# Performance work log

Measured on AMD Instinct MI355X. Metric: run time of the kernel, lower is better.

The kernel has to match this reference:

```python
import math
import jax, jax.numpy as jnp
import numpy as np

FACTOR = 1  # init factor; top_k = max(1, int(FACTOR * log(L)))


def setup_inputs() -> dict:
    key = jax.random.key(0)
    kq, kk, kv = jax.random.split(key, 3)
    B, L, H, E = 8, 4096, 8, 64
    queries = jax.random.normal(kq, (B, L, H, E), dtype=jnp.float32)
    keys = jax.random.normal(kk, (B, L, H, E), dtype=jnp.float32)
    values = jax.random.normal(kv, (B, L, H, E), dtype=jnp.float32)
    return {"queries": queries, "keys": keys, "values": values}


def reference(queries, keys, values):
    # queries/keys: [B, L, H, E], values: [B, L, H, D] (L == S so no padding branch)
    B, L, H, E = queries.shape
    q = jnp.transpose(queries, (0, 2, 3, 1))  # [B, H, E, L]
    k = jnp.transpose(keys, (0, 2, 3, 1))
    v = jnp.transpose(values, (0, 2, 3, 1))   # [B, H, D, L]

    # FFT-based circular cross-correlation along time axis
    qf = jnp.fft.rfft(q, axis=-1)
    kf = jnp.fft.rfft(k, axis=-1)
    corr = jnp.fft.irfft(qf * jnp.conj(kf), n=L, axis=-1)  # [B, H, E, L]

    # Inference-time delay aggregation (eval path of the module)
    top_k = max(1, int(FACTOR * math.log(L)))
    mean_corr = corr.mean(axis=(1, 2))                      # [B, L]
    w_top, idx_top = jax.lax.top_k(mean_corr, top_k)        # [B, K]
    w = jax.nn.softmax(w_top, axis=-1)                      # [B, K]

    # circular shift: out[..., t] = sum_i w_i * v[..., (t + delay_i) mod L]
    t = jnp.arange(L)
    idx = (t[None, None, :] + idx_top[:, :, None]) % L      # [B, K, L]
    gathered = jnp.take_along_axis(
        v[:, None], idx[:, :, None, None, :], axis=-1
    )                                                       # [B, K, H, D, L]
    agg = jnp.einsum('bkhdl,bk->bhdl', gathered, w)         # [B, H, D, L]
    return jnp.transpose(agg, (0, 3, 1, 2))                 # [B, L, H, D]
```

## Files before the change

kernel.cpp:

```cpp
#include <hip/hip_runtime.h>
#include <math.h>


namespace {
constexpr int LEN  = 4096;
constexpr int HALF = 2048;
constexpr int NCH  = 512;
constexpr int NB   = 8;
constexpr int KTOP = 8;
constexpr int TPB  = 256;
constexpr int CPB  = 8;
constexpr int GPB  = NCH / CPB;
constexpr size_t SF_BYTES = (size_t)NB * LEN * 2 * sizeof(float);
constexpr size_t WI_BYTES = (size_t)NB * KTOP * sizeof(float);
constexpr size_t ZT_OFF   = SF_BYTES + 2 * WI_BYTES;
constexpr size_t ZT_BYTES = (size_t)NB * NCH * LEN * 2 * sizeof(float);
}

__device__ __forceinline__ void fft4096_fwd(float2* __restrict__ bufA,
                                            float2* __restrict__ bufB,
                                            const float2* __restrict__ tw,
                                            int tid)
{
  float2* src = bufA;
  float2* dst = bufB;
  #pragma unroll
  for (int st = 0; st < 12; ++st) {
    const int s = 1 << st;
    #pragma unroll
    for (int r = 0; r < HALF / TPB; ++r) {
      const int j = tid + r * TPB;
      const int q = j & (s - 1);
      const int p = j >> st;
      const float2 a = src[j];
      const float2 b = src[j + HALF];
      const float2 w = tw[j - q];
      const float dx = a.x - b.x, dy = a.y - b.y;
      const int o0 = j + s * p;
      dst[o0]     = make_float2(a.x + b.x, a.y + b.y);
      dst[o0 + s] = make_float2(dx * w.x - dy * w.y, dx * w.y + dy * w.x);
    }
    __syncthreads();
    float2* t_ = src; src = dst; dst = t_;
  }
}

__global__ __launch_bounds__(TPB) void k_transpose(
    const float* __restrict__ qg, const float* __restrict__ kg,
    float2* __restrict__ zt)
{
  __shared__ float2 tile[64 * 65];
  const int bt  = blockIdx.x;
  const int b   = bt >> 9;
  const int t0  = ((bt >> 3) & 63) * 64;
  const int c0  = (bt & 7) * 64;
  const int tid = threadIdx.x;
  const size_t base = (size_t)b * LEN * NCH;

  #pragma unroll
  for (int r = 0; r < 16; ++r) {
    const int idx  = r * TPB + tid;
    const int ch_l = idx & 63;
    const int t_l  = idx >> 6;
    const size_t g = base + (size_t)(t0 + t_l) * NCH + (c0 + ch_l);
    tile[t_l * 65 + ch_l] = make_float2(qg[g], kg[g]);
  }
  __syncthreads();
  #pragma unroll
  for (int r = 0; r < 16; ++r) {
    const int idx  = r * TPB + tid;
    const int t_l  = idx & 63;
    const int ch_l = idx >> 6;
    zt[((size_t)b * NCH + (c0 + ch_l)) * LEN + (t0 + t_l)] =
        tile[t_l * 65 + ch_l];
  }
}

__global__ __launch_bounds__(TPB) void k_fft_corr(
    const float2* __restrict__ zt,
    float* __restrict__ Sf)
{
  __shared__ float2 bufA[LEN];
  __shared__ float2 bufB[LEN];
  __shared__ float2 tw[HALF];
  const int tid = threadIdx.x;
  const int b   = blockIdx.x / GPB;
  const int g   = blockIdx.x % GPB;
  const int ch0 = g * CPB;

  for (int t = tid; t < HALF; t += TPB) {
    float s, c;
    __sincosf((float)t * (float)(-2.0 * M_PI / 4096.0), &s, &c);
    tw[t] = make_float2(c, s);
  }

  float2 acc[LEN / TPB];
  #pragma unroll
  for (int r = 0; r < LEN / TPB; ++r) acc[r] = make_float2(0.f, 0.f);

  for (int cc = 0; cc < CPB; ++cc) {
    const float2* src = zt + ((size_t)b * NCH + (ch0 + cc)) * LEN;
    __syncthreads();
    #pragma unroll
    for (int r = 0; r < LEN / TPB; ++r) {
      const int t = tid + r * TPB;
      bufA[t] = src[t];
    }
    __syncthreads();
    fft4096_fwd(bufA, bufB, tw, tid);
    #pragma unroll
    for (int r = 0; r < LEN / TPB; ++r) {
      const int f = tid + r * TPB;
      const float2 A  = bufA[f];
      float2 Bv = bufA[(LEN - f) & (LEN - 1)];
      Bv.y = -Bv.y;
      const float Sx = A.x + Bv.x, Sy = A.y + Bv.y;
      const float Dx = A.x - Bv.x, Dy = -(A.y - Bv.y);
      const float Mx = Sx * Dx - Sy * Dy;
      const float My = Sx * Dy + Sy * Dx;
      acc[r].x += -0.25f * My;
      acc[r].y +=  0.25f * Mx;
    }
  }
  float* dstp = Sf + (size_t)b * LEN * 2;
  #pragma unroll
  for (int r = 0; r < LEN / TPB; ++r) {
    const int f = tid + r * TPB;
    atomicAdd(&dstp[2 * f],     acc[r].x);
    atomicAdd(&dstp[2 * f + 1], acc[r].y);
  }
}

__global__ __launch_bounds__(TPB) void k_fft_corr_strided(
    const float* __restrict__ qg, const float* __restrict__ kg,
    float* __restrict__ Sf)
{
  __shared__ float2 bufA[LEN];
  __shared__ float2 bufB[LEN];
  __shared__ float2 tw[HALF];
  const int tid = threadIdx.x;
  const int b   = blockIdx.x / GPB;
  const int g   = blockIdx.x % GPB;
  const int ch0 = g * CPB;

  for (int t = tid; t < HALF; t += TPB) {
    float s, c;
    __sincosf((float)t * (float)(-2.0 * M_PI / 4096.0), &s, &c);
    tw[t] = make_float2(c, s);
  }
  float2 acc[LEN / TPB];
  #pragma unroll
  for (int r = 0; r < LEN / TPB; ++r) acc[r] = make_float2(0.f, 0.f);

  const size_t base = (size_t)b * LEN * NCH;
  for (int cc = 0; cc < CPB; ++cc) {
    const int ch = ch0 + cc;
    __syncthreads();
    #pragma unroll
    for (int r = 0; r < LEN / TPB; ++r) {
      const int t = tid + r * TPB;
      const size_t idx = base + (size_t)t * NCH + ch;
      bufA[t] = make_float2(qg[idx], kg[idx]);
    }
    __syncthreads();
    fft4096_fwd(bufA, bufB, tw, tid);
    #pragma unroll
    for (int r = 0; r < LEN / TPB; ++r) {
      const int f = tid + r * TPB;
      const float2 A  = bufA[f];
      float2 Bv = bufA[(LEN - f) & (LEN - 1)];
      Bv.y = -Bv.y;
      const float Sx = A.x + Bv.x, Sy = A.y + Bv.y;
      const float Dx = A.x - Bv.x, Dy = -(A.y - Bv.y);
      const float Mx = Sx * Dx - Sy * Dy;
      const float My = Sx * Dy + Sy * Dx;
      acc[r].x += -0.25f * My;
      acc[r].y +=  0.25f * Mx;
    }
  }
  float* dstp = Sf + (size_t)b * LEN * 2;
  #pragma unroll
  for (int r = 0; r < LEN / TPB; ++r) {
    const int f = tid + r * TPB;
    atomicAdd(&dstp[2 * f],     acc[r].x);
    atomicAdd(&dstp[2 * f + 1], acc[r].y);
  }
}

__global__ __launch_bounds__(TPB) void k_ifft_topk(
    const float* __restrict__ Sf,
    float* __restrict__ wout, int* __restrict__ iout)
{
  __shared__ float2 bufA[LEN];
  __shared__ float2 bufB[LEN];
  __shared__ float2 tw[HALF];
  __shared__ float  R[LEN];
  __shared__ float  rv[TPB];
  __shared__ int    ri[TPB];
  __shared__ float  topv[KTOP];
  __shared__ int    topi[KTOP];
  const int tid = threadIdx.x;
  const int b   = blockIdx.x;

  for (int t = tid; t < HALF; t += TPB) {
    float s, c;
    __sincosf((float)t * (float)(-2.0 * M_PI / 4096.0), &s, &c);
    tw[t] = make_float2(c, s);
  }
  const float* srcp = Sf + (size_t)b * LEN * 2;
  for (int r = 0; r < LEN / TPB; ++r) {
    const int f = tid + r * TPB;
    bufA[f] = make_float2(srcp[2 * f], -srcp[2 * f + 1]);
  }
  __syncthreads();
  fft4096_fwd(bufA, bufB, tw, tid);
  const float scale = 1.0f / (4096.0f * 512.0f);
  for (int r = 0; r < LEN / TPB; ++r) {
    const int f = tid + r * TPB;
    R[f] = bufA[f].x * scale;
  }
  __syncthreads();

  for (int it = 0; it < KTOP; ++it) {
    float best = -INFINITY; int bi = 0;
    for (int r = 0; r < LEN / TPB; ++r) {
      const int f = tid + r * TPB;
      const float v = R[f];
      if (v > best) { best = v; bi = f; }
    }
    rv[tid] = best; ri[tid] = bi;
    __syncthreads();
    for (int off = TPB / 2; off > 0; off >>= 1) {
      if (tid < off && rv[tid + off] > rv[tid]) {
        rv[tid] = rv[tid + off]; ri[tid] = ri[tid + off];
      }
      __syncthreads();
    }
    if (tid == 0) {
      topv[it] = rv[0]; topi[it] = ri[0];
      R[ri[0]] = -INFINITY;
    }
    __syncthreads();
  }
  if (tid == 0) {
    const float m = topv[0];
    float e[KTOP], den = 0.f;
    for (int i = 0; i < KTOP; ++i) { e[i] = expf(topv[i] - m); den += e[i]; }
    for (int i = 0; i < KTOP; ++i) {
      wout[b * KTOP + i] = e[i] / den;
      iout[b * KTOP + i] = topi[i];
    }
  }
}

__global__ __launch_bounds__(256) void k_gather(
    const float4* __restrict__ v, const float* __restrict__ wk,
    const int* __restrict__ ik, float4* __restrict__ out)
{
  __shared__ float sw[KTOP];
  __shared__ int   sidx[KTOP];
  const int b  = blockIdx.x >> 11;
  const int tp = blockIdx.x & 2047;
  if (threadIdx.x < KTOP) {
    sw[threadIdx.x]   = wk[b * KTOP + threadIdx.x];
    sidx[threadIdx.x] = ik[b * KTOP + threadIdx.x];
  }
  __syncthreads();
  const int t = tp * 2 + (threadIdx.x >> 7);
  const int c = threadIdx.x & 127;
  const size_t vbase = (size_t)b * LEN * 128;
  float4 acc = make_float4(0.f, 0.f, 0.f, 0.f);
  #pragma unroll
  for (int i = 0; i < KTOP; ++i) {
    const int st = (t + sidx[i]) & (LEN - 1);
    const float4 x = v[vbase + (size_t)st * 128 + c];
    acc.x += sw[i] * x.x; acc.y += sw[i] * x.y;
    acc.z += sw[i] * x.z; acc.w += sw[i] * x.w;
  }
  out[vbase + (size_t)t * 128 + c] = acc;
}

extern "C" void kernel_launch(void* const* d_in, const int* in_sizes, int n_in,
                              void* d_out, int out_size, void* d_ws, size_t ws_size,
                              hipStream_t stream) {
  const float* q = (const float*)d_in[0];
  const float* k = (const float*)d_in[1];
  const float* v = (const float*)d_in[2];
  float* out = (float*)d_out;

  float*  Sf = (float*)d_ws;
  float*  wk = (float*)((char*)d_ws + SF_BYTES);
  int*    ik = (int*)((char*)d_ws + SF_BYTES + WI_BYTES);
  float2* zt = (float2*)((char*)d_ws + ZT_OFF);

  hipMemsetAsync(d_ws, 0, SF_BYTES, stream);
  if (ws_size >= ZT_OFF + ZT_BYTES) {
    k_transpose<<<NB * 64 * 8, TPB, 0, stream>>>(q, k, zt);
    k_fft_corr<<<NB * GPB, TPB, 0, stream>>>(zt, Sf);
  } else {
    k_fft_corr_strided<<<NB * GPB, TPB, 0, stream>>>(q, k, Sf);
  }
  k_ifft_topk<<<NB, TPB, 0, stream>>>(Sf, wk, ik);
  k_gather<<<NB * 2048, 256, 0, stream>>>((const float4*)v, wk, ik,
                                          (float4*)out);
}
```

Measured before the change: 413.2 us.

## Replace radix-2 Stockham FFT with in-place radix-16 three-pass FFT

```diff
diff --git a/kernel.cpp b/kernel.cpp
--- a/kernel.cpp
+++ b/kernel.cpp
@@ -4,45 +4,117 @@
 
 namespace {
 constexpr int LEN  = 4096;
-constexpr int HALF = 2048;
 constexpr int NCH  = 512;
 constexpr int NB   = 8;
 constexpr int KTOP = 8;
 constexpr int TPB  = 256;
-constexpr int CPB  = 8;
+constexpr int CPB  = 4;
 constexpr int GPB  = NCH / CPB;
 constexpr size_t SF_BYTES = (size_t)NB * LEN * 2 * sizeof(float);
 constexpr size_t WI_BYTES = (size_t)NB * KTOP * sizeof(float);
 constexpr size_t ZT_OFF   = SF_BYTES + 2 * WI_BYTES;
 constexpr size_t ZT_BYTES = (size_t)NB * NCH * LEN * 2 * sizeof(float);
-}
-
-__device__ __forceinline__ void fft4096_fwd(float2* __restrict__ bufA,
-                                            float2* __restrict__ bufB,
-                                            const float2* __restrict__ tw,
-                                            int tid)
-{
-  float2* src = bufA;
-  float2* dst = bufB;
-  #pragma unroll
-  for (int st = 0; st < 12; ++st) {
-    const int s = 1 << st;
-    #pragma unroll
-    for (int r = 0; r < HALF / TPB; ++r) {
-      const int j = tid + r * TPB;
-      const int q = j & (s - 1);
-      const int p = j >> st;
-      const float2 a = src[j];
-      const float2 b = src[j + HALF];
-      const float2 w = tw[j - q];
-      const float dx = a.x - b.x, dy = a.y - b.y;
-      const int o0 = j + s * p;
-      dst[o0]     = make_float2(a.x + b.x, a.y + b.y);
-      dst[o0 + s] = make_float2(dx * w.x - dy * w.y, dx * w.y + dy * w.x);
-    }
-    __syncthreads();
-    float2* t_ = src; src = dst; dst = t_;
-  }
+constexpr int PADN = LEN + (LEN >> 4);
+}
+
+#define PD(i) ((i) + ((i) >> 4))
+
+__device__ __forceinline__ float2 cmul(float2 a, float2 b) {
+  return make_float2(a.x * b.x - a.y * b.y, a.x * b.y + a.y * b.x);
+}
+
+__device__ __forceinline__ void dft16(const float2* __restrict__ a,
+                                      float2* __restrict__ b) {
+  const float C1 = 0.92387953251128674f;
+  const float S1 = 0.38268343236508978f;
+  const float R2 = 0.70710678118654752f;
+  float2 c[4][4];
+  #pragma unroll
+  for (int r0 = 0; r0 < 4; ++r0) {
+    const float2 x0 = a[r0], x1 = a[4 + r0], x2 = a[8 + r0], x3 = a[12 + r0];
+    const float2 s02 = make_float2(x0.x + x2.x, x0.y + x2.y);
+    const float2 d02 = make_float2(x0.x - x2.x, x0.y - x2.y);
+    const float2 s13 = make_float2(x1.x + x3.x, x1.y + x3.y);
+    const float2 d13 = make_float2(x1.x - x3.x, x1.y - x3.y);
+    c[r0][0] = make_float2(s02.x + s13.x, s02.y + s13.y);
+    c[r0][2] = make_float2(s02.x - s13.x, s02.y - s13.y);
+    c[r0][1] = make_float2(d02.x + d13.y, d02.y - d13.x);
+    c[r0][3] = make_float2(d02.x - d13.y, d02.y + d13.x);
+  }
+  #pragma unroll
+  for (int k0 = 0; k0 < 4; ++k0) {
+    float2 t0 = c[0][k0], t1 = c[1][k0], t2 = c[2][k0], t3 = c[3][k0];
+    if (k0 == 1) {
+      t1 = cmul(t1, make_float2(C1, -S1));
+      t2 = cmul(t2, make_float2(R2, -R2));
+      t3 = cmul(t3, make_float2(S1, -C1));
+    } else if (k0 == 2) {
+      t1 = cmul(t1, make_float2(R2, -R2));
+      t2 = make_float2(t2.y, -t2.x);
+      t3 = cmul(t3, make_float2(-R2, -R2));
+    } else if (k0 == 3) {
+      t1 = cmul(t1, make_float2(S1, -C1));
+      t2 = cmul(t2, make_float2(-R2, -R2));
+      t3 = cmul(t3, make_float2(-C1, S1));
+    }
+    const float2 s02 = make_float2(t0.x + t2.x, t0.y + t2.y);
+    const float2 d02 = make_float2(t0.x - t2.x, t0.y - t2.y);
+    const float2 s13 = make_float2(t1.x + t3.x, t1.y + t3.y);
+    const float2 d13 = make_float2(t1.x - t3.x, t1.y - t3.y);
+    b[k0]      = make_float2(s02.x + s13.x, s02.y + s13.y);
+    b[k0 + 8]  = make_float2(s02.x - s13.x, s02.y - s13.y);
+    b[k0 + 4]  = make_float2(d02.x + d13.y, d02.y - d13.x);
+    b[k0 + 12] = make_float2(d02.x - d13.y, d02.y + d13.x);
+  }
+}
+
+__device__ __forceinline__ void fft4096_ip(float2* __restrict__ buf, int tid)
+{
+  float2 a[16], b[16];
+  const float NEG2PI_N = -6.283185307179586f / 4096.0f;
+  {
+    #pragma unroll
+    for (int r = 0; r < 16; ++r) a[r] = buf[PD(tid + 256 * r)];
+    dft16(a, b);
+    float sn, cs;
+    __sincosf((float)tid * NEG2PI_N, &sn, &cs);
+    const float2 w1 = make_float2(cs, sn);
+    __syncthreads();
+    float2 w = make_float2(1.f, 0.f);
+    #pragma unroll
+    for (int k = 0; k < 16; ++k) {
+      buf[PD(16 * tid + k)] = cmul(b[k], w);
+      w = cmul(w, w1);
+    }
+  }
+  __syncthreads();
+  {
+    const int q = tid & 15, p = tid >> 4;
+    #pragma unroll
+    for (int r = 0; r < 16; ++r) a[r] = buf[PD(tid + 256 * r)];
+    dft16(a, b);
+    float sn, cs;
+    __sincosf((float)(16 * p) * NEG2PI_N, &sn, &cs);
+    const float2 w1 = make_float2(cs, sn);
+    __syncthreads();
+    float2 w = make_float2(1.f, 0.f);
+    const int ob = q + 256 * p;
+    #pragma unroll
+    for (int k = 0; k < 16; ++k) {
+      buf[PD(ob + 16 * k)] = cmul(b[k], w);
+      w = cmul(w, w1);
+    }
+  }
+  __syncthreads();
+  {
+    #pragma unroll
+    for (int r = 0; r < 16; ++r) a[r] = buf[PD(tid + 256 * r)];
+    dft16(a, b);
+    __syncthreads();
+    #pragma unroll
+    for (int k = 0; k < 16; ++k) buf[PD(tid + 256 * k)] = b[k];
+  }
+  __syncthreads();
 }
 
 __global__ __launch_bounds__(TPB) void k_transpose(
@@ -76,56 +148,57 @@
   }
 }
 
+__device__ __forceinline__ void spec_acc(const float2* __restrict__ buf,
+                                         int tid, float2* __restrict__ acc)
+{
+  #pragma unroll
+  for (int r = 0; r < 16; ++r) {
+    const int f = tid + 256 * r;
+    const float2 A = buf[PD(f)];
+    float2 Bv = buf[PD((LEN - f) & (LEN - 1))];
+    Bv.y = -Bv.y;
+    const float Sx = A.x + Bv.x, Sy = A.y + Bv.y;
+    const float Dx = A.x - Bv.x, Dy = -(A.y - Bv.y);
+    const float Mx = Sx * Dx - Sy * Dy;
+    const float My = Sx * Dy + Sy * Dx;
+    acc[r].x += -0.25f * My;
+    acc[r].y +=  0.25f * Mx;
+  }
+}
+
 __global__ __launch_bounds__(TPB) void k_fft_corr(
     const float2* __restrict__ zt,
     float* __restrict__ Sf)
 {
-  __shared__ float2 bufA[LEN];
-  __shared__ float2 bufB[LEN];
-  __shared__ float2 tw[HALF];
+  __shared__ float2 buf[PADN];
   const int tid = threadIdx.x;
   const int b   = blockIdx.x / GPB;
   const int g   = blockIdx.x % GPB;
   const int ch0 = g * CPB;
 
-  for (int t = tid; t < HALF; t += TPB) {
-    float s, c;
-    __sincosf((float)t * (float)(-2.0 * M_PI / 4096.0), &s, &c);
-    tw[t] = make_float2(c, s);
-  }
-
-  float2 acc[LEN / TPB];
-  #pragma unroll
-  for (int r = 0; r < LEN / TPB; ++r) acc[r] = make_float2(0.f, 0.f);
+  float2 acc[16];
+  #pragma unroll
+  for (int r = 0; r < 16; ++r) acc[r] = make_float2(0.f, 0.f);
 
   for (int cc = 0; cc < CPB; ++cc) {
-    const float2* src = zt + ((size_t)b * NCH + (ch0 + cc)) * LEN;
-    __syncthreads();
-    #pragma unroll
-    for (int r = 0; r < LEN / TPB; ++r) {
-      const int t = tid + r * TPB;
-      bufA[t] = src[t];
-    }
-    __syncthreads();
-    fft4096_fwd(bufA, bufB, tw, tid);
-    #pragma unroll
-    for (int r = 0; r < LEN / TPB; ++r) {
-      const int f = tid + r * TPB;
-      const float2 A  = bufA[f];
-      float2 Bv = bufA[(LEN - f) & (LEN - 1)];
-      Bv.y = -Bv.y;
-      const float Sx = A.x + Bv.x, Sy = A.y + Bv.y;
-      const float Dx = A.x - Bv.x, Dy = -(A.y - Bv.y);
-      const float Mx = Sx * Dx - Sy * Dy;
-      const float My = Sx * Dy + Sy * Dx;
-      acc[r].x += -0.25f * My;
-      acc[r].y +=  0.25f * Mx;
-    }
+    const float4* src =
+        (const float4*)(zt + ((size_t)b * NCH + (ch0 + cc)) * LEN);
+    #pragma unroll
+    for (int r = 0; r < 8; ++r) {
+      const float4 x = src[tid + 256 * r];
+      const int t = 2 * (tid + 256 * r);
+      buf[PD(t)]     = make_float2(x.x, x.y);
+      buf[PD(t + 1)] = make_float2(x.z, x.w);
+    }
+    __syncthreads();
+    fft4096_ip(buf, tid);
+    spec_acc(buf, tid, acc);
+    __syncthreads();
   }
   float* dstp = Sf + (size_t)b * LEN * 2;
   #pragma unroll
-  for (int r = 0; r < LEN / TPB; ++r) {
-    const int f = tid + r * TPB;
+  for (int r = 0; r < 16; ++r) {
+    const int f = tid + 256 * r;
     atomicAdd(&dstp[2 * f],     acc[r].x);
     atomicAdd(&dstp[2 * f + 1], acc[r].y);
   }
@@ -135,53 +208,34 @@
     const float* __restrict__ qg, const float* __restrict__ kg,
     float* __restrict__ Sf)
 {
-  __shared__ float2 bufA[LEN];
-  __shared__ float2 bufB[LEN];
-  __shared__ float2 tw[HALF];
+  __shared__ float2 buf[PADN];
   const int tid = threadIdx.x;
   const int b   = blockIdx.x / GPB;
   const int g   = blockIdx.x % GPB;
   const int ch0 = g * CPB;
 
-  for (int t = tid; t < HALF; t += TPB) {
-    float s, c;
-    __sincosf((float)t * (float)(-2.0 * M_PI / 4096.0), &s, &c);
-    tw[t] = make_float2(c, s);
-  }
-  float2 acc[LEN / TPB];
-  #pragma unroll
-  for (int r = 0; r < LEN / TPB; ++r) acc[r] = make_float2(0.f, 0.f);
+  float2 acc[16];
+  #pragma unroll
+  for (int r = 0; r < 16; ++r) acc[r] = make_float2(0.f, 0.f);
 
   const size_t base = (size_t)b * LEN * NCH;
   for (int cc = 0; cc < CPB; ++cc) {
     const int ch = ch0 + cc;
-    __syncthreads();
-    #pragma unroll
-    for (int r = 0; r < LEN / TPB; ++r) {
-      const int t = tid + r * TPB;
+    #pragma unroll
+    for (int r = 0; r < 16; ++r) {
+      const int t = tid + 256 * r;
       const size_t idx = base + (size_t)t * NCH + ch;
-      bufA[t] = make_float2(qg[idx], kg[idx]);
-    }
-    __syncthreads();
-    fft4096_fwd(bufA, bufB, tw, tid);
-    #pragma unroll
-    for (int r = 0; r < LEN / TPB; ++r) {
-      const int f = tid + r * TPB;
-      const float2 A  = bufA[f];
-      float2 Bv = bufA[(LEN - f) & (LEN - 1)];
-      Bv.y = -Bv.y;
-      const float Sx = A.x + Bv.x, Sy = A.y + Bv.y;
-      const float Dx = A.x - Bv.x, Dy = -(A.y - Bv.y);
-      const float Mx = Sx * Dx - Sy * Dy;
-      const float My = Sx * Dy + Sy * Dx;
-      acc[r].x += -0.25f * My;
-      acc[r].y +=  0.25f * Mx;
-    }
+      buf[PD(t)] = make_float2(qg[idx], kg[idx]);
+    }
+    __syncthreads();
+    fft4096_ip(buf, tid);
+    spec_acc(buf, tid, acc);
+    __syncthreads();
   }
   float* dstp = Sf + (size_t)b * LEN * 2;
   #pragma unroll
-  for (int r = 0; r < LEN / TPB; ++r) {
-    const int f = tid + r * TPB;
+  for (int r = 0; r < 16; ++r) {
+    const int f = tid + 256 * r;
     atomicAdd(&dstp[2 * f],     acc[r].x);
     atomicAdd(&dstp[2 * f + 1], acc[r].y);
   }
@@ -191,61 +245,69 @@
     const float* __restrict__ Sf,
     float* __restrict__ wout, int* __restrict__ iout)
 {
-  __shared__ float2 bufA[LEN];
-  __shared__ float2 bufB[LEN];
-  __shared__ float2 tw[HALF];
-  __shared__ float  R[LEN];
-  __shared__ float  rv[TPB];
-  __shared__ int    ri[TPB];
-  __shared__ float  topv[KTOP];
-  __shared__ int    topi[KTOP];
+  __shared__ float2 buf[PADN];
+  __shared__ float swv[4];
+  __shared__ int   swi[4];
+  __shared__ int   gsel;
+  __shared__ float topv[KTOP];
+  __shared__ int   topi[KTOP];
   const int tid = threadIdx.x;
   const int b   = blockIdx.x;
 
-  for (int t = tid; t < HALF; t += TPB) {
-    float s, c;
-    __sincosf((float)t * (float)(-2.0 * M_PI / 4096.0), &s, &c);
-    tw[t] = make_float2(c, s);
-  }
-  const float* srcp = Sf + (size_t)b * LEN * 2;
-  for (int r = 0; r < LEN / TPB; ++r) {
-    const int f = tid + r * TPB;
-    bufA[f] = make_float2(srcp[2 * f], -srcp[2 * f + 1]);
-  }
-  __syncthreads();
-  fft4096_fwd(bufA, bufB, tw, tid);
+  const float2* srcp = (const float2*)Sf + (size_t)b * LEN;
+  #pragma unroll
+  for (int r = 0; r < 16; ++r) {
+    const int f = tid + 256 * r;
+    const float2 s = srcp[f];
+    buf[PD(f)] = make_float2(s.x, -s.y);
+  }
+  __syncthreads();
+  fft4096_ip(buf, tid);
+
   const float scale = 1.0f / (4096.0f * 512.0f);
-  for (int r = 0; r < LEN / TPB; ++r) {
-    const int f = tid + r * TPB;
-    R[f] = bufA[f].x * scale;
-  }
-  __syncthreads();
-
+  float rv[16];
+  #pragma unroll
+  for (int r = 0; r < 16; ++r) rv[r] = buf[PD(tid + 256 * r)].x * scale;
+
+  const int lane = tid & 63, wv = tid >> 6;
   for (int it = 0; it < KTOP; ++it) {
-    float best = -INFINITY; int bi = 0;
-    for (int r = 0; r < LEN / TPB; ++r) {
-      const int f = tid + r * TPB;
-      const float v = R[f];
-      if (v > best) { best = v; bi = f; }
-    }
-    rv[tid] = best; ri[tid] = bi;
-    __syncthreads();
-    for (int off = TPB / 2; off > 0; off >>= 1) {
-      if (tid < off && rv[tid + off] > rv[tid]) {
-        rv[tid] = rv[tid + off]; ri[tid] = ri[tid + off];
-      }
-      __syncthreads();
-    }
+    float best = -INFINITY;
+    int   bi   = 0x7fffffff;
+    #pragma unroll
+    for (int r = 0; r < 16; ++r) {
+      if (rv[r] > best) { best = rv[r]; bi = tid + 256 * r; }
+    }
+    #pragma unroll
+    for (int off = 32; off > 0; off >>= 1) {
+      const float ov = __shfl_xor(best, off);
+      const int   oi = __shfl_xor(bi, off);
+      if (ov > best || (ov == best && oi < bi)) { best = ov; bi = oi; }
+    }
+    if (lane == 0) { swv[wv] = best; swi[wv] = bi; }
+    __syncthreads();
     if (tid == 0) {
-      topv[it] = rv[0]; topi[it] = ri[0];
-      R[ri[0]] = -INFINITY;
-    }
-    __syncthreads();
+      float gv = swv[0]; int gi = swi[0];
+      for (int w2 = 1; w2 < 4; ++w2)
+        if (swv[w2] > gv || (swv[w2] == gv && swi[w2] < gi)) {
+          gv = swv[w2]; gi = swi[w2];
+        }
+      topv[it] = gv; topi[it] = gi; gsel = gi;
+    }
+    __syncthreads();
+    const int gi = gsel;
+    if ((gi & 255) == tid) {
+      const int rr = gi >> 8;
+      #pragma unroll
+      for (int r = 0; r < 16; ++r)
+        if (r == rr) rv[r] = -INFINITY;
+    }
   }
   if (tid == 0) {
     const float m = topv[0];
     float e[KTOP], den = 0.f;
+    #pragma unroll
     for (int i = 0; i < KTOP; ++i) { e[i] = expf(topv[i] - m); den += e[i]; }
+    #pragma unroll
     for (int i = 0; i < KTOP; ++i) {
       wout[b * KTOP + i] = e[i] / den;
       iout[b * KTOP + i] = topi[i];
@@ -286,7 +348,6 @@
   const float* q = (const float*)d_in[0];
   const float* k = (const float*)d_in[1];
   const float* v = (const float*)d_in[2];
-  float* out = (float*)d_out;
 
   float*  Sf = (float*)d_ws;
   float*  wk = (float*)((char*)d_ws + SF_BYTES);
@@ -302,5 +363,5 @@
   }
   k_ifft_topk<<<NB, TPB, 0, stream>>>(Sf, wk, ik);
   k_gather<<<NB * 2048, 256, 0, stream>>>((const float4*)v, wk, ik,
-                                          (float4*)out);
-}
+                                          (float4*)(float*)d_out);
+}
```

Measured after the change: 403.4 us. 2.4% less time.
